# Kernel tuning notes

Hardware: AMD Instinct MI355X
Metric: run time of the kernel (lower is better)

## Reference

```python
import jax, jax.numpy as jnp
import numpy as np

B, S, TK, H, E, V, OOV = 16, 8, 400, 256, 128, 50000, 50
H2 = 2 * H


def setup_inputs() -> dict:
    key = jax.random.key(0)
    ks = jax.random.split(key, 24)
    std = 0.02
    d = {}
    d["y_t_1"] = jax.random.randint(ks[0], (B,), 0, V)
    d["h0"] = jax.random.normal(ks[1], (B, H), jnp.float32)
    d["c0"] = jax.random.normal(ks[2], (B, H), jnp.float32)
    d["encoder_output"] = jax.random.normal(ks[3], (B, S, TK, H2), jnp.float32)
    d["section_output"] = jax.random.normal(ks[4], (B, S, H2), jnp.float32)
    d["enc_padding_mask"] = jnp.ones((B, S, TK), jnp.float32)
    d["c_t_1"] = jax.random.normal(ks[5], (B, H2), jnp.float32)
    d["extra_zeros"] = jnp.zeros((B, OOV), jnp.float32)
    d["enc_batch_extend_vocab"] = jax.random.randint(ks[6], (B, S * TK), 0, V + OOV)
    d["coverage"] = jnp.zeros((B, S, TK), jnp.float32)
    d["gamma"] = jnp.ones((B, S, TK), jnp.float32)
    # learned parameters
    d["embedding"] = std * jax.random.normal(ks[7], (V, E), jnp.float32)
    d["W_xc"] = std * jax.random.normal(ks[8], (H2 + E, E), jnp.float32)
    d["b_xc"] = jnp.zeros((E,), jnp.float32)
    d["W_ih"] = std * jax.random.normal(ks[9], (E, 4 * H), jnp.float32)
    d["b_ih"] = jnp.zeros((4 * H,), jnp.float32)
    d["W_hh"] = std * jax.random.normal(ks[10], (H, 4 * H), jnp.float32)
    # pytorch init sets forget-gate bias (2nd quarter) to 1
    d["b_hh"] = jnp.zeros((4 * H,), jnp.float32).at[H:2 * H].set(1.0)
    d["Wh_sec"] = std * jax.random.normal(ks[11], (H2, H2), jnp.float32)
    d["Wd_sec"] = std * jax.random.normal(ks[12], (H2, H2), jnp.float32)
    d["bd_sec"] = jnp.zeros((H2,), jnp.float32)
    d["v_sec"] = std * jax.random.normal(ks[13], (H2, 1), jnp.float32)
    d["Wh_w"] = std * jax.random.normal(ks[14], (H2, H2), jnp.float32)
    d["Wc_w"] = std * jax.random.normal(ks[15], (H2,), jnp.float32)
    d["Wd_w"] = std * jax.random.normal(ks[16], (H2, H2), jnp.float32)
    d["bd_w"] = jnp.zeros((H2,), jnp.float32)
    d["v_w"] = std * jax.random.normal(ks[17], (H2, 1), jnp.float32)
    d["W_pgen"] = std * jax.random.normal(ks[18], (4 * H + E, 1), jnp.float32)
    d["b_pgen"] = jnp.zeros((1,), jnp.float32)
    d["W_out1"] = std * jax.random.normal(ks[19], (3 * H, H), jnp.float32)
    d["b_out1"] = jnp.zeros((H,), jnp.float32)
    d["W_out2"] = std * jax.random.normal(ks[20], (H, V), jnp.float32)
    d["b_out2"] = jnp.zeros((V,), jnp.float32)
    return d


def reference(y_t_1, h0, c0, encoder_output, section_output, enc_padding_mask,
              c_t_1, extra_zeros, enc_batch_extend_vocab, coverage, gamma,
              embedding, W_xc, b_xc, W_ih, b_ih, W_hh, b_hh,
              Wh_sec, Wd_sec, bd_sec, v_sec,
              Wh_w, Wc_w, Wd_w, bd_w, v_w,
              W_pgen, b_pgen, W_out1, b_out1, W_out2, b_out2):
    # embedding + input context projection
    emb = embedding[y_t_1]                                      # [B,E]
    x = jnp.concatenate([c_t_1, emb], axis=1) @ W_xc + b_xc     # [B,E]
    # single-step LSTM (pytorch gate order i,f,g,o)
    gates = x @ W_ih + b_ih + h0 @ W_hh + b_hh                  # [B,4H]
    i, f, g, o = jnp.split(gates, 4, axis=1)
    c = jax.nn.sigmoid(f) * c0 + jax.nn.sigmoid(i) * jnp.tanh(g)
    h = jax.nn.sigmoid(o) * jnp.tanh(c)
    s_t_hat = jnp.concatenate([h, c], axis=1)                   # [B,2H]
    # section attention -> beta [B,S]
    e_sec = jnp.tanh(section_output @ Wh_sec + (s_t_hat @ Wd_sec + bd_sec)[:, None, :])
    sc_sec = jnp.squeeze(e_sec @ v_sec, -1)                     # [B,S]
    beta = jax.nn.softmax(sc_sec, axis=1)
    beta = beta / beta.sum(axis=1, keepdims=True)
    # word attention with coverage feature
    att = encoder_output @ Wh_w + (s_t_hat @ Wd_w + bd_w)[:, None, None, :]
    att = att + coverage[..., None] * Wc_w                      # [B,S,TK,2H]
    sc_w = jnp.squeeze(jnp.tanh(att) @ v_w, -1)                 # [B,S,TK]
    ws = (beta[:, :, None] * sc_w).reshape(B, S * TK)
    mask = enc_padding_mask.reshape(B, S * TK)
    ad = jax.nn.softmax(ws, axis=1) * mask
    attn = ad / ad.sum(axis=1, keepdims=True)                   # [B,S*TK]
    c_t = jnp.einsum('bt,btn->bn', attn, encoder_output.reshape(B, S * TK, H2))
    cov = coverage + attn.reshape(B, S, TK)
    # pointer-gen gate
    p_gen = jax.nn.sigmoid(jnp.concatenate([c_t, s_t_hat, x], axis=1) @ W_pgen + b_pgen)  # [B,1]
    # output vocab distribution
    out = jnp.concatenate([h, c_t], axis=1) @ W_out1 + b_out1
    vocab_dist = jax.nn.softmax(out @ W_out2 + b_out2, axis=1)  # [B,V]
    vd = jnp.concatenate([p_gen * vocab_dist, extra_zeros], axis=1)  # [B,V+OOV]
    ad_ = (1.0 - p_gen) * attn
    rows = jnp.arange(B)[:, None]
    final_dist = vd.at[rows, enc_batch_extend_vocab].add(ad_)
    return (final_dist, h, c, c_t, attn, p_gen, cov)
```

## Files before the change

### kernel.cpp

```cpp
#include <hip/hip_runtime.h>
#include <math.h>

#define BB   16
#define SS   8
#define TKK  400
#define HH   256
#define EE   128
#define VV   50000
#define OOVV 50
#define HH2  512
#define STK  (SS*TKK)
#define VOO  (VV+OOVV)

#define OFF_X     0
#define OFF_ST    2048
#define OFF_SD    10240
#define OFF_WD    18432
#define OFF_SCSEC 26752
#define OFF_SCW   26880
#define OFF_CT    78080
#define OFF_OUT1  86272
#define OFF_PGEN  90368
#define OFF_PSUM  93520
#define OFF_BT    113040

#define O_FD   0
#define O_H    800800
#define O_C    804896
#define O_CT   808992
#define O_ATTN 817184
#define O_PGEN 868384
#define O_COV  868400

#define NLBLK 782
#define GEMM_NB 800

typedef __attribute__((ext_vector_type(8))) short bf16x8;
typedef __attribute__((ext_vector_type(4))) float f32x4;

__device__ __forceinline__ float sigm(float x){ return 1.0f/(1.0f+expf(-x)); }

__device__ __forceinline__ unsigned short f2b(float f){
  unsigned int u = __float_as_uint(f);
  unsigned int r = (u + 0x7fffu + ((u >> 16) & 1u)) >> 16;
  return (unsigned short)r;
}

__device__ __forceinline__ float wave_sum(float v){
  #pragma unroll
  for(int o=32;o>0;o>>=1) v += __shfl_xor(v,o);
  return v;
}
__device__ __forceinline__ float wave_max(float v){
  #pragma unroll
  for(int o=32;o>0;o>>=1) v = fmaxf(v,__shfl_xor(v,o));
  return v;
}

__global__ void k_pre(const float* __restrict__ Whw, unsigned short* __restrict__ Btg,
                      const int* __restrict__ y, const float* __restrict__ ct1,
                      const float* __restrict__ emb, const float* __restrict__ Wxc,
                      const float* __restrict__ bxc, float* __restrict__ ws){
  __shared__ float sm[10440];
  int bi = blockIdx.x, tid = threadIdx.x;
  if(bi < 64){
    int n0 = (bi & 7)*64, k0 = (bi >> 3)*64;
    int tx = tid & 63, ty = tid >> 6;
    #pragma unroll
    for(int it=0; it<16; it++){
      int kk = it*4 + ty;
      sm[kk*65 + tx] = Whw[(size_t)(k0+kk)*HH2 + n0 + tx];
    }
    __syncthreads();
    #pragma unroll
    for(int it=0; it<2; it++){
      int kgl = it*4 + ty;
      int kgG = (k0 >> 3) + kgl;
      union{ bf16x8 v; unsigned short u[8]; } t;
      #pragma unroll
      for(int j=0;j<8;j++) t.u[j] = f2b(sm[(kgl*8+j)*65 + tx]);
      *(bf16x8*)&Btg[((size_t)kgG*HH2 + n0 + tx)*8] = t.v;
    }
  } else if(bi < 80){
    float* cat = sm;
    float* red = sm + 10240;
    for(int f=tid; f<BB*640; f+=256){
      int b = f/640, r = f - b*640;
      cat[f] = (r < HH2) ? ct1[b*HH2 + r] : emb[(size_t)y[b]*EE + (r-HH2)];
    }
    __syncthreads();
    int c = (bi-64)*8 + (tid & 7);
    int b = (tid >> 3) & 15;
    int kh = tid >> 7;
    float acc = 0.0f;
    const float* a = &cat[b*640];
    for(int k=kh*320; k<kh*320+320; k++) acc += a[k]*Wxc[k*EE + c];
    if(kh==1) red[b*8 + (tid&7)] = acc;
    __syncthreads();
    if(kh==0) ws[OFF_X + b*EE + c] = acc + red[b*8 + (tid&7)] + bxc[c];
  } else {
    for(int f=tid; f<BB*HH2; f+=256) ws[OFF_CT + f] = 0.0f;
  }
}

__global__ void k_lstm(const float* __restrict__ h0, const float* __restrict__ c0,
                       const float* __restrict__ Wih, const float* __restrict__ bih,
                       const float* __restrict__ Whh, const float* __restrict__ bhh,
                       float* __restrict__ ws, float* __restrict__ out){
  __shared__ float xh[4*384];
  __shared__ float red[3*64*4];
  int tid = threadIdx.x;
  int jc = (blockIdx.x & 15)*16, bc = (blockIdx.x >> 4)*4;
  for(int f=tid; f<4*384; f+=256){
    int bl = f/384, r = f - bl*384;
    xh[f] = (r < EE) ? ws[OFF_X + (bc+bl)*EE + r] : h0[(bc+bl)*HH + (r-EE)];
  }
  __syncthreads();
  int jl = tid & 15, bl = (tid >> 4) & 3, kq = tid >> 6;
  int j = jc + jl, b = bc + bl;
  float a0=0.f, a1=0.f, a2=0.f, a3=0.f;
  const float* a = &xh[bl*384];
  for(int k=kq*96; k<kq*96+96; k++){
    float v = a[k];
    const float* w = (k < EE) ? &Wih[k*4*HH + j] : &Whh[(k-EE)*4*HH + j];
    a0 += v*w[0]; a1 += v*w[HH]; a2 += v*w[2*HH]; a3 += v*w[3*HH];
  }
  if(kq){
    float* r = &red[((kq-1)*64 + bl*16 + jl)*4];
    r[0]=a0; r[1]=a1; r[2]=a2; r[3]=a3;
  }
  __syncthreads();
  if(kq==0){
    #pragma unroll
    for(int p=0;p<3;p++){
      const float* r = &red[(p*64 + bl*16 + jl)*4];
      a0+=r[0]; a1+=r[1]; a2+=r[2]; a3+=r[3];
    }
    a0 += bih[j] + bhh[j];
    a1 += bih[j+HH] + bhh[j+HH];
    a2 += bih[j+2*HH] + bhh[j+2*HH];
    a3 += bih[j+3*HH] + bhh[j+3*HH];
    float c = sigm(a1)*c0[b*HH+j] + sigm(a0)*tanhf(a2);
    float h = sigm(a3)*tanhf(c);
    out[O_H + b*HH + j] = h;
    out[O_C + b*HH + j] = c;
    ws[OFF_ST + b*HH2 + j]      = h;
    ws[OFF_ST + b*HH2 + HH + j] = c;
  }
}

__global__ void k_proj(const float* __restrict__ Wdsec, const float* __restrict__ bdsec,
                       const float* __restrict__ Wdw,  const float* __restrict__ bdw,
                       float* __restrict__ ws){
  __shared__ float st[BB*HH2];
  __shared__ float red[128];
  int tid = threadIdx.x;
  for(int f=tid; f<BB*HH2; f+=256) st[f] = ws[OFF_ST + f];
  __syncthreads();
  int mi = blockIdx.x >> 6;
  int c = (blockIdx.x & 63)*8 + (tid & 7);
  int bl = (tid >> 3) & 15;
  int kq = tid >> 7;
  const float* Wm = mi ? Wdw : Wdsec;
  const float* bias = mi ? bdw : bdsec;
  int dst = mi ? OFF_WD : OFF_SD;
  float acc = 0.0f;
  const float* a = &st[bl*HH2];
  for(int k=kq*256; k<kq*256+256; k++) acc += a[k]*Wm[k*HH2 + c];
  if(kq==1) red[bl*8 + (tid&7)] = acc;
  __syncthreads();
  if(kq==0) ws[dst + bl*HH2 + c] = acc + red[bl*8 + (tid&7)] + bias[c];
}

__global__ __launch_bounds__(512, 4) void k_gemm6(
        const float* __restrict__ A, const unsigned short* __restrict__ Btg,
        const float* __restrict__ Wcw, const float* __restrict__ vw,
        const float* __restrict__ cover,
        const float* __restrict__ sec, const float* __restrict__ Whsec,
        const float* __restrict__ vsec, float* __restrict__ ws){
  __shared__ __align__(16) unsigned short smem[18432];
  int tid = threadIdx.x;
  if(blockIdx.x >= GEMM_NB){
    float* row = (float*)smem;
    float* red = row + HH2;
    int bi = blockIdx.x - GEMM_NB;
    int b = bi >> 3;
    if(tid < HH2) row[tid] = sec[(size_t)bi*HH2 + tid];
    __syncthreads();
    int col = tid;
    float acc = 0.0f;
    #pragma unroll 8
    for(int k=0;k<HH2;k++) acc += row[k]*Whsec[k*HH2 + col];
    float val = tanhf(acc + ws[OFF_SD + b*HH2 + col]) * vsec[col];
    val = wave_sum(val);
    if((tid&63)==0) red[tid>>6] = val;
    __syncthreads();
    if(tid==0){
      float s = 0.0f;
      #pragma unroll
      for(int i=0;i<8;i++) s += red[i];
      ws[OFF_SCSEC + bi] = s;
    }
    return;
  }
  unsigned short* As = smem;
  unsigned short* Bs = smem + 2048;
  int w = tid >> 6, lane = tid & 63, m = lane & 15, q = lane >> 4;
  int mk = (m >> 1) & 3;
  int rg = w >> 1, cg = w & 1;
  int row0 = blockIdx.x * 64;
  int b = blockIdx.x / 50;
  float cov[4];
  #pragma unroll
  for(int r=0;r<4;r++) cov[r] = cover[row0 + rg*16 + q*4 + r];
  f32x4 acc[16];
  #pragma unroll
  for(int j=0;j<16;j++) acc[j] = (f32x4){0.f,0.f,0.f,0.f};

  int arow = tid >> 2, akg = tid & 3;
  int bcol = tid;

  for(int rnd=0; rnd<16; rnd++){
    int k0 = rnd*32;
    if(tid < 256){
      const float4* src = (const float4*)&A[(size_t)(row0+arow)*HH2 + k0 + akg*8];
      float4 v0 = src[0], v1 = src[1];
      union{ bf16x8 v; unsigned short u[8]; } t;
      t.u[0]=f2b(v0.x); t.u[1]=f2b(v0.y); t.u[2]=f2b(v0.z); t.u[3]=f2b(v0.w);
      t.u[4]=f2b(v1.x); t.u[5]=f2b(v1.y); t.u[6]=f2b(v1.z); t.u[7]=f2b(v1.w);
      *(bf16x8*)&As[(arow*4 + (akg ^ ((arow>>1)&3)))*8] = t.v;
    }
    #pragma unroll
    for(int i=0;i<4;i++){
      bf16x8 bv = *(const bf16x8*)&Btg[((size_t)(rnd*4+i)*HH2 + bcol)*8];
      *(bf16x8*)&Bs[(bcol*4 + (i ^ ((bcol>>1)&3)))*8] = bv;
    }
    __syncthreads();
    bf16x8 af = *(bf16x8*)&As[((rg*16+m)*4 + (q ^ mk))*8];
    #pragma unroll
    for(int j=0;j<16;j++){
      int col = cg*256 + j*16 + m;
      bf16x8 bfv = *(bf16x8*)&Bs[(col*4 + (q ^ mk))*8];
      acc[j] = __builtin_amdgcn_mfma_f32_16x16x32_bf16(af, bfv, acc[j], 0,0,0);
    }
    __syncthreads();
  }
  float rsum[4] = {0,0,0,0};
  #pragma unroll
  for(int j=0;j<16;j++){
    int col = cg*256 + j*16 + m;
    float wdv = ws[OFF_WD + b*HH2 + col];
    float wcv = Wcw[col], vwv = vw[col];
    #pragma unroll
    for(int r=0;r<4;r++)
      rsum[r] += tanhf(acc[j][r] + wdv + cov[r]*wcv) * vwv;
  }
  float* rbuf = (float*)smem;
  #pragma unroll
  for(int r=0;r<4;r++){
    float v = rsum[r];
    v += __shfl_xor(v,1,16); v += __shfl_xor(v,2,16);
    v += __shfl_xor(v,4,16); v += __shfl_xor(v,8,16);
    if(m==0) rbuf[cg*64 + rg*16 + q*4 + r] = v;
  }
  __syncthreads();
  if(tid < 64) ws[OFF_SCW + row0 + tid] = rbuf[tid] + rbuf[64 + tid];
}

__global__ void k_attn(const float* __restrict__ mask, const float* __restrict__ cover,
                       float* __restrict__ ws, float* __restrict__ out){
  int b = blockIdx.x, tid = threadIdx.x;
  __shared__ float vals[STK];
  __shared__ float red[4];
  __shared__ float sc[SS];
  if(tid < SS) sc[tid] = ws[OFF_SCSEC + b*SS + tid];
  __syncthreads();
  float bm = -1e30f;
  #pragma unroll
  for(int s=0;s<SS;s++) bm = fmaxf(bm, sc[s]);
  float be[SS]; float bsum = 0.0f;
  #pragma unroll
  for(int s=0;s<SS;s++){ be[s] = expf(sc[s]-bm); bsum += be[s]; }
  #pragma unroll
  for(int s=0;s<SS;s++) be[s] /= bsum;
  int lane = tid & 63, w = tid >> 6;
  float m = -1e30f;
  for(int j=tid;j<STK;j+=256){
    float v = be[j/TKK] * ws[OFF_SCW + b*STK + j];
    vals[j] = v; m = fmaxf(m, v);
  }
  m = wave_max(m);
  if(lane==0) red[w] = m;
  __syncthreads();
  m = fmaxf(fmaxf(red[0],red[1]), fmaxf(red[2],red[3]));
  __syncthreads();
  float ssum = 0.0f;
  for(int j=tid;j<STK;j+=256){
    float e = expf(vals[j]-m) * mask[b*STK + j];
    vals[j] = e; ssum += e;
  }
  ssum = wave_sum(ssum);
  if(lane==0) red[w] = ssum;
  __syncthreads();
  float inv = 1.0f/(red[0]+red[1]+red[2]+red[3]);
  for(int j=tid;j<STK;j+=256){
    float a = vals[j]*inv;
    out[O_ATTN + b*STK + j] = a;
    out[O_COV  + b*STK + j] = cover[b*STK + j] + a;
  }
}

__global__ void k_ct(const float* __restrict__ enc, const float* __restrict__ out,
                     float* __restrict__ ws){
  int b = blockIdx.y, tid = threadIdx.x;
  __shared__ float a[64];
  int t0 = blockIdx.x*64;
  if(tid<64) a[tid] = out[O_ATTN + b*STK + t0 + tid];
  __syncthreads();
  float acc0=0.0f, acc1=0.0f;
  #pragma unroll 4
  for(int tt=0;tt<64;tt++){
    const float* row = &enc[(size_t)(b*STK + t0 + tt)*HH2];
    float av = a[tt];
    acc0 += av*row[tid];
    acc1 += av*row[256+tid];
  }
  atomicAdd(&ws[OFF_CT + b*HH2 + tid],       acc0);
  atomicAdd(&ws[OFF_CT + b*HH2 + 256 + tid], acc1);
}

__global__ void k_out1(const float* __restrict__ Wp, const float* __restrict__ bp,
                       const float* __restrict__ Wo1, const float* __restrict__ bo1,
                       float* __restrict__ ws, float* __restrict__ out){
  __shared__ float cat[BB*768];
  __shared__ float red[3*64];
  int tid = threadIdx.x;
  if(blockIdx.x == 64){
    int w = tid >> 6, lane = tid & 63;
    #pragma unroll
    for(int i=0;i<4;i++){
      int b = w*4 + i;
      float p = 0.0f;
      for(int k=lane;k<4*HH+EE;k+=64){
        float val = (k < HH2) ? ws[OFF_CT + b*HH2 + k]
                  : (k < 4*HH) ? ws[OFF_ST + b*HH2 + (k-HH2)]
                  : ws[OFF_X + b*EE + (k-4*HH)];
        p += val * Wp[k];
      }
      p = wave_sum(p);
      if(lane==0){
        float pg = sigm(p + bp[0]);
        ws[OFF_PGEN + b] = pg;
        out[O_PGEN + b]  = pg;
      }
    }
    for(int f=tid; f<BB*HH2; f+=256) out[O_CT + f] = ws[OFF_CT + f];
    return;
  }
  for(int f=tid; f<BB*768; f+=256){
    int b = f/768, r = f - b*768;
    cat[f] = (r < HH) ? ws[OFF_ST + b*HH2 + r] : ws[OFF_CT + b*HH2 + (r-HH)];
  }
  __syncthreads();
  int cl = tid & 3, bl = (tid >> 2) & 15, kq = tid >> 6;
  int c = blockIdx.x*4 + cl;
  float acc = 0.0f;
  const float* a = &cat[bl*768];
  for(int k=kq*192; k<kq*192+192; k++) acc += a[k]*Wo1[k*HH + c];
  if(kq) red[(kq-1)*64 + bl*4 + cl] = acc;
  __syncthreads();
  if(kq==0){
    acc += red[bl*4+cl] + red[64 + bl*4+cl] + red[128 + bl*4+cl];
    ws[OFF_OUT1 + bl*HH + c] = acc + bo1[c];
  }
}

__global__ void k_logits(const float* __restrict__ W2, const float* __restrict__ b2,
                         float* __restrict__ ws, float* __restrict__ out){
  int tid = threadIdx.x;
  int c = blockIdx.x*64 + (tid & 63);
  int bq = tid >> 6;
  __shared__ float o1[BB*HH];
  for(int i=tid;i<BB*HH;i+=256) o1[i] = ws[OFF_OUT1 + i];
  __syncthreads();
  bool ok = c < VV;
  float acc[4] = {0,0,0,0};
  if(ok){
    for(int k=0;k<HH;k++){
      float wv = W2[(size_t)k*VV + c];
      #pragma unroll
      for(int i=0;i<4;i++) acc[i] += o1[(bq*4+i)*HH + k]*wv;
    }
  }
  float bias = ok ? b2[c] : 0.0f;
  int lane = tid & 63;
  #pragma unroll
  for(int i=0;i<4;i++){
    float e = ok ? expf(acc[i]+bias) : 0.0f;
    if(ok) out[(size_t)(bq*4+i)*VOO + c] = e;
    float sv = wave_sum(e);
    if(lane==0) ws[OFF_PSUM + blockIdx.x*BB + bq*4 + i] = sv;
  }
}

__global__ void k_final(const float* __restrict__ xz, float* __restrict__ ws,
                        float* __restrict__ out){
  int b = blockIdx.y;
  int v = blockIdx.x*256 + threadIdx.x;
  __shared__ float red[4];
  int lane = threadIdx.x & 63, w = threadIdx.x >> 6;
  float p = 0.0f;
  for(int i=threadIdx.x;i<NLBLK;i+=256) p += ws[OFF_PSUM + i*BB + b];
  p = wave_sum(p);
  if(lane==0) red[w] = p;
  __syncthreads();
  float s = red[0]+red[1]+red[2]+red[3];
  float pg = ws[OFF_PGEN + b];
  if(v < VV)       out[(size_t)b*VOO + v] = pg * out[(size_t)b*VOO + v] / s;
  else if(v < VOO) out[(size_t)b*VOO + v] = xz[b*OOVV + (v-VV)];
}

__global__ void k_scatter(const int* __restrict__ ebev, float* __restrict__ ws,
                          float* __restrict__ out){
  int b = blockIdx.x;
  float r = 1.0f - ws[OFF_PGEN + b];
  for(int j=threadIdx.x;j<STK;j+=256){
    int idx = ebev[b*STK + j];
    atomicAdd(&out[(size_t)b*VOO + idx], r*out[O_ATTN + b*STK + j]);
  }
}

extern "C" void kernel_launch(void* const* d_in, const int* in_sizes, int n_in,
                              void* d_out, int out_size, void* d_ws, size_t ws_size,
                              hipStream_t stream){
  const int*   y     = (const int*)  d_in[0];
  const float* h0    = (const float*)d_in[1];
  const float* c0    = (const float*)d_in[2];
  const float* enc   = (const float*)d_in[3];
  const float* sec   = (const float*)d_in[4];
  const float* mask  = (const float*)d_in[5];
  const float* ct1   = (const float*)d_in[6];
  const float* xz    = (const float*)d_in[7];
  const int*   ebev  = (const int*)  d_in[8];
  const float* cover = (const float*)d_in[9];
  const float* emb   = (const float*)d_in[11];
  const float* Wxc   = (const float*)d_in[12];
  const float* bxc   = (const float*)d_in[13];
  const float* Wih   = (const float*)d_in[14];
  const float* bih   = (const float*)d_in[15];
  const float* Whh   = (const float*)d_in[16];
  const float* bhh   = (const float*)d_in[17];
  const float* Whsec = (const float*)d_in[18];
  const float* Wdsec = (const float*)d_in[19];
  const float* bdsec = (const float*)d_in[20];
  const float* vsec  = (const float*)d_in[21];
  const float* Whw   = (const float*)d_in[22];
  const float* Wcw   = (const float*)d_in[23];
  const float* Wdw   = (const float*)d_in[24];
  const float* bdw   = (const float*)d_in[25];
  const float* vw    = (const float*)d_in[26];
  const float* Wp    = (const float*)d_in[27];
  const float* bp    = (const float*)d_in[28];
  const float* Wo1   = (const float*)d_in[29];
  const float* bo1   = (const float*)d_in[30];
  const float* Wo2   = (const float*)d_in[31];
  const float* bo2   = (const float*)d_in[32];
  float* out = (float*)d_out;
  float* ws  = (float*)d_ws;
  unsigned short* Btg = (unsigned short*)(ws + OFF_BT);

  k_pre    <<<dim3(81),       dim3(256), 0, stream>>>(Whw, Btg, y, ct1, emb, Wxc, bxc, ws);
  k_lstm   <<<dim3(64),       dim3(256), 0, stream>>>(h0, c0, Wih, bih, Whh, bhh, ws, out);
  k_proj   <<<dim3(128),      dim3(256), 0, stream>>>(Wdsec, bdsec, Wdw, bdw, ws);
  k_gemm6  <<<dim3(928),      dim3(512), 0, stream>>>(enc, Btg, Wcw, vw, cover, sec, Whsec, vsec, ws);
  k_attn   <<<dim3(BB),       dim3(256), 0, stream>>>(mask, cover, ws, out);
  k_ct     <<<dim3(50,BB),    dim3(256), 0, stream>>>(enc, out, ws);
  k_out1   <<<dim3(65),       dim3(256), 0, stream>>>(Wp, bp, Wo1, bo1, ws, out);
  k_logits <<<dim3(NLBLK),    dim3(256), 0, stream>>>(Wo2, bo2, ws, out);
  k_final  <<<dim3(196,BB),   dim3(256), 0, stream>>>(xz, ws, out);
  k_scatter<<<dim3(BB),       dim3(256), 0, stream>>>(ebev, ws, out);
}
```

Before: 498.8 us.

## Pipeline attention GEMM with async LDS loads and vectorize ct and logits kernels

The attention GEMM now double-buffers pre-swizzled B tiles through direct global-to-LDS loads, and feeds A fragments from registers with a prefetch of the next k-slice. k_pre writes the weight in the swizzled layout this requires. A fast clamped exp-based tanh replaces tanhf in the GEMM epilogue. k_ct and k_logits switch to float4 loads, and k_logits uses half as many blocks with a batch-major partial-sum layout. The aim is to hide memory latency and cut instruction overhead, at the cost of a larger LDS footprint, less accurate tanh, and hand-tuned waitcnt logic that is fragile.

```diff
diff --git a/kernel.cpp b/kernel.cpp
--- a/kernel.cpp
+++ b/kernel.cpp
@@ -32,7 +32,7 @@
 #define O_PGEN 868384
 #define O_COV  868400
 
-#define NLBLK 782
+#define NLB 391
 #define GEMM_NB 800
 
 typedef __attribute__((ext_vector_type(8))) short bf16x8;
@@ -46,6 +46,12 @@
   return (unsigned short)r;
 }
 
+__device__ __forceinline__ float tanhfast(float x){
+  float cx = fminf(9.0f, fmaxf(-9.0f, x));
+  float t = __expf(2.0f*cx);
+  return (t - 1.0f) * __builtin_amdgcn_rcpf(t + 1.0f);
+}
+
 __device__ __forceinline__ float wave_sum(float v){
   #pragma unroll
   for(int o=32;o>0;o>>=1) v += __shfl_xor(v,o);
@@ -55,6 +61,18 @@
   #pragma unroll
   for(int o=32;o>0;o>>=1) v = fmaxf(v,__shfl_xor(v,o));
   return v;
+}
+
+__device__ __forceinline__ void glds16(const void* g, void* l){
+  __builtin_amdgcn_global_load_lds((const __attribute__((address_space(1))) void*)g,
+                                   (__attribute__((address_space(3))) void*)l, 16, 0, 0);
+}
+
+__device__ __forceinline__ bf16x8 cvt8(float4 a, float4 b){
+  union{ bf16x8 v; unsigned short u[8]; } t;
+  t.u[0]=f2b(a.x); t.u[1]=f2b(a.y); t.u[2]=f2b(a.z); t.u[3]=f2b(a.w);
+  t.u[4]=f2b(b.x); t.u[5]=f2b(b.y); t.u[6]=f2b(b.z); t.u[7]=f2b(b.w);
+  return t.v;
 }
 
 __global__ void k_pre(const float* __restrict__ Whw, unsigned short* __restrict__ Btg,
@@ -76,10 +94,12 @@
     for(int it=0; it<2; it++){
       int kgl = it*4 + ty;
       int kgG = (k0 >> 3) + kgl;
+      int rnd = kgG >> 2, kg = kgG & 3;
+      int col = n0 + tx;
       union{ bf16x8 v; unsigned short u[8]; } t;
       #pragma unroll
       for(int j=0;j<8;j++) t.u[j] = f2b(sm[(kgl*8+j)*65 + tx]);
-      *(bf16x8*)&Btg[((size_t)kgG*HH2 + n0 + tx)*8] = t.v;
+      *(bf16x8*)&Btg[(size_t)rnd*16384 + (size_t)(col*4 + (kg ^ ((col>>1)&3)))*8] = t.v;
     }
   } else if(bi < 80){
     float* cat = sm;
@@ -178,7 +198,7 @@
         const float* __restrict__ cover,
         const float* __restrict__ sec, const float* __restrict__ Whsec,
         const float* __restrict__ vsec, float* __restrict__ ws){
-  __shared__ __align__(16) unsigned short smem[18432];
+  __shared__ __align__(16) unsigned short smem[32768];
   int tid = threadIdx.x;
   if(blockIdx.x >= GEMM_NB){
     float* row = (float*)smem;
@@ -203,48 +223,67 @@
     }
     return;
   }
-  unsigned short* As = smem;
-  unsigned short* Bs = smem + 2048;
   int w = tid >> 6, lane = tid & 63, m = lane & 15, q = lane >> 4;
-  int mk = (m >> 1) & 3;
+  int mk = (m >> 1) & 3, sw = q ^ mk;
   int rg = w >> 1, cg = w & 1;
   int row0 = blockIdx.x * 64;
   int b = blockIdx.x / 50;
+
+  const float* arow_p = &A[(size_t)(row0 + rg*16 + m)*HH2 + q*8];
+
+  f32x4 acc[16];
+  #pragma unroll
+  for(int j=0;j<16;j++) acc[j] = (f32x4){0.f,0.f,0.f,0.f};
+
+  #define GLDSB(rr, bufsel) {                                                  \
+    const unsigned short* bsrc_ = Btg + (size_t)(rr)*16384;                    \
+    _Pragma("unroll")                                                          \
+    for(int i_=0;i_<4;i_++)                                                    \
+      glds16(bsrc_ + i_*4096 + tid*8, &smem[(bufsel)*16384 + i_*4096 + tid*8]);\
+  }
+
+  GLDSB(0, 0);
+  float4 pa0 = *(const float4*)(arow_p);
+  float4 pa1 = *(const float4*)(arow_p + 4);
+  GLDSB(1, 1);
+  asm volatile("s_waitcnt vmcnt(6)" ::: "memory");
+  __builtin_amdgcn_sched_barrier(0);
+  bf16x8 af = cvt8(pa0, pa1);
+  __builtin_amdgcn_s_barrier();
+
+  #pragma unroll
+  for(int r=0; r<16; r++){
+    if(r < 15){
+      pa0 = *(const float4*)(arow_p + (r+1)*32);
+      pa1 = *(const float4*)(arow_p + (r+1)*32 + 4);
+    }
+    __builtin_amdgcn_s_setprio(1);
+    #pragma unroll
+    for(int cf=0; cf<16; cf++){
+      int col = cg*256 + cf*16 + m;
+      bf16x8 bv = *(const bf16x8*)&smem[(size_t)(r&1)*16384 + ((size_t)col*4 + sw)*8];
+      acc[cf] = __builtin_amdgcn_mfma_f32_16x16x32_bf16(af, bv, acc[cf], 0,0,0);
+    }
+    __builtin_amdgcn_s_setprio(0);
+    if(r < 14){
+      asm volatile("s_waitcnt lgkmcnt(0)" ::: "memory");
+      __builtin_amdgcn_sched_barrier(0);
+      __builtin_amdgcn_s_barrier();
+      GLDSB(r+2, (r&1));
+    }
+    if(r < 15){
+      if(r < 14){ asm volatile("s_waitcnt vmcnt(6)" ::: "memory"); }
+      else      { asm volatile("s_waitcnt vmcnt(2)" ::: "memory"); }
+      __builtin_amdgcn_sched_barrier(0);
+      af = cvt8(pa0, pa1);
+      __builtin_amdgcn_s_barrier();
+    }
+  }
+  #undef GLDSB
+
   float cov[4];
   #pragma unroll
   for(int r=0;r<4;r++) cov[r] = cover[row0 + rg*16 + q*4 + r];
-  f32x4 acc[16];
-  #pragma unroll
-  for(int j=0;j<16;j++) acc[j] = (f32x4){0.f,0.f,0.f,0.f};
-
-  int arow = tid >> 2, akg = tid & 3;
-  int bcol = tid;
-
-  for(int rnd=0; rnd<16; rnd++){
-    int k0 = rnd*32;
-    if(tid < 256){
-      const float4* src = (const float4*)&A[(size_t)(row0+arow)*HH2 + k0 + akg*8];
-      float4 v0 = src[0], v1 = src[1];
-      union{ bf16x8 v; unsigned short u[8]; } t;
-      t.u[0]=f2b(v0.x); t.u[1]=f2b(v0.y); t.u[2]=f2b(v0.z); t.u[3]=f2b(v0.w);
-      t.u[4]=f2b(v1.x); t.u[5]=f2b(v1.y); t.u[6]=f2b(v1.z); t.u[7]=f2b(v1.w);
-      *(bf16x8*)&As[(arow*4 + (akg ^ ((arow>>1)&3)))*8] = t.v;
-    }
-    #pragma unroll
-    for(int i=0;i<4;i++){
-      bf16x8 bv = *(const bf16x8*)&Btg[((size_t)(rnd*4+i)*HH2 + bcol)*8];
-      *(bf16x8*)&Bs[(bcol*4 + (i ^ ((bcol>>1)&3)))*8] = bv;
-    }
-    __syncthreads();
-    bf16x8 af = *(bf16x8*)&As[((rg*16+m)*4 + (q ^ mk))*8];
-    #pragma unroll
-    for(int j=0;j<16;j++){
-      int col = cg*256 + j*16 + m;
-      bf16x8 bfv = *(bf16x8*)&Bs[(col*4 + (q ^ mk))*8];
-      acc[j] = __builtin_amdgcn_mfma_f32_16x16x32_bf16(af, bfv, acc[j], 0,0,0);
-    }
-    __syncthreads();
-  }
   float rsum[4] = {0,0,0,0};
   #pragma unroll
   for(int j=0;j<16;j++){
@@ -253,8 +292,9 @@
     float wcv = Wcw[col], vwv = vw[col];
     #pragma unroll
     for(int r=0;r<4;r++)
-      rsum[r] += tanhf(acc[j][r] + wdv + cov[r]*wcv) * vwv;
-  }
+      rsum[r] += tanhfast(acc[j][r] + wdv + cov[r]*wcv) * vwv;
+  }
+  __syncthreads();
   float* rbuf = (float*)smem;
   #pragma unroll
   for(int r=0;r<4;r++){
@@ -314,19 +354,29 @@
                      float* __restrict__ ws){
   int b = blockIdx.y, tid = threadIdx.x;
   __shared__ float a[64];
+  __shared__ float part[512];
   int t0 = blockIdx.x*64;
   if(tid<64) a[tid] = out[O_ATTN + b*STK + t0 + tid];
   __syncthreads();
-  float acc0=0.0f, acc1=0.0f;
-  #pragma unroll 4
-  for(int tt=0;tt<64;tt++){
-    const float* row = &enc[(size_t)(b*STK + t0 + tt)*HH2];
-    float av = a[tt];
-    acc0 += av*row[tid];
-    acc1 += av*row[256+tid];
-  }
-  atomicAdd(&ws[OFF_CT + b*HH2 + tid],       acc0);
-  atomicAdd(&ws[OFF_CT + b*HH2 + 256 + tid], acc1);
+  int c4 = tid & 127, rh = tid >> 7;
+  const float4* e4 = (const float4*)enc;
+  size_t base = ((size_t)(b*STK + t0 + rh*32))*128 + c4;
+  float4 acc = {0.f,0.f,0.f,0.f};
+  #pragma unroll 8
+  for(int rr=0; rr<32; rr++){
+    float4 v = e4[base + (size_t)rr*128];
+    float av = a[rh*32 + rr];
+    acc.x += av*v.x; acc.y += av*v.y; acc.z += av*v.z; acc.w += av*v.w;
+  }
+  if(rh) *(float4*)&part[c4*4] = acc;
+  __syncthreads();
+  if(!rh){
+    float4 o = *(const float4*)&part[c4*4];
+    atomicAdd(&ws[OFF_CT + b*HH2 + c4*4 + 0], acc.x + o.x);
+    atomicAdd(&ws[OFF_CT + b*HH2 + c4*4 + 1], acc.y + o.y);
+    atomicAdd(&ws[OFF_CT + b*HH2 + c4*4 + 2], acc.z + o.z);
+    atomicAdd(&ws[OFF_CT + b*HH2 + c4*4 + 3], acc.w + o.w);
+  }
 }
 
 __global__ void k_out1(const float* __restrict__ Wp, const float* __restrict__ bp,
@@ -378,28 +428,46 @@
 __global__ void k_logits(const float* __restrict__ W2, const float* __restrict__ b2,
                          float* __restrict__ ws, float* __restrict__ out){
   int tid = threadIdx.x;
-  int c = blockIdx.x*64 + (tid & 63);
-  int bq = tid >> 6;
   __shared__ float o1[BB*HH];
-  for(int i=tid;i<BB*HH;i+=256) o1[i] = ws[OFF_OUT1 + i];
-  __syncthreads();
-  bool ok = c < VV;
-  float acc[4] = {0,0,0,0};
+  for(int i=tid;i<BB*HH/4;i+=256)
+    ((float4*)o1)[i] = ((const float4*)&ws[OFF_OUT1])[i];
+  __syncthreads();
+  int cl = tid & 31, bq = tid >> 5;
+  int c4 = blockIdx.x*128 + cl*4;
+  bool ok = c4 < VV;
+  int b0 = bq*2, b1 = b0+1;
+  float4 acc0 = {0.f,0.f,0.f,0.f}, acc1 = {0.f,0.f,0.f,0.f};
   if(ok){
+    const float* oa = &o1[b0*HH];
+    const float* ob = &o1[b1*HH];
+    #pragma unroll 4
     for(int k=0;k<HH;k++){
-      float wv = W2[(size_t)k*VV + c];
-      #pragma unroll
-      for(int i=0;i<4;i++) acc[i] += o1[(bq*4+i)*HH + k]*wv;
-    }
-  }
-  float bias = ok ? b2[c] : 0.0f;
-  int lane = tid & 63;
-  #pragma unroll
-  for(int i=0;i<4;i++){
-    float e = ok ? expf(acc[i]+bias) : 0.0f;
-    if(ok) out[(size_t)(bq*4+i)*VOO + c] = e;
-    float sv = wave_sum(e);
-    if(lane==0) ws[OFF_PSUM + blockIdx.x*BB + bq*4 + i] = sv;
+      float4 wv = *(const float4*)&W2[(size_t)k*VV + c4];
+      float xa = oa[k], xb = ob[k];
+      acc0.x += xa*wv.x; acc0.y += xa*wv.y; acc0.z += xa*wv.z; acc0.w += xa*wv.w;
+      acc1.x += xb*wv.x; acc1.y += xb*wv.y; acc1.z += xb*wv.z; acc1.w += xb*wv.w;
+    }
+  }
+  float bv[4] = {0,0,0,0};
+  if(ok){ float4 t = *(const float4*)&b2[c4]; bv[0]=t.x; bv[1]=t.y; bv[2]=t.z; bv[3]=t.w; }
+  float a0[4] = {acc0.x, acc0.y, acc0.z, acc0.w};
+  float a1[4] = {acc1.x, acc1.y, acc1.z, acc1.w};
+  float s0 = 0.0f, s1 = 0.0f;
+  #pragma unroll
+  for(int j=0;j<4;j++){
+    float e0 = ok ? expf(a0[j]+bv[j]) : 0.0f;
+    float e1 = ok ? expf(a1[j]+bv[j]) : 0.0f;
+    if(ok){
+      out[(size_t)b0*VOO + c4 + j] = e0;
+      out[(size_t)b1*VOO + c4 + j] = e1;
+    }
+    s0 += e0; s1 += e1;
+  }
+  #pragma unroll
+  for(int o=1;o<32;o<<=1){ s0 += __shfl_xor(s0,o,32); s1 += __shfl_xor(s1,o,32); }
+  if(cl==0){
+    ws[OFF_PSUM + b0*NLB + blockIdx.x] = s0;
+    ws[OFF_PSUM + b1*NLB + blockIdx.x] = s1;
   }
 }
 
@@ -410,7 +478,7 @@
   __shared__ float red[4];
   int lane = threadIdx.x & 63, w = threadIdx.x >> 6;
   float p = 0.0f;
-  for(int i=threadIdx.x;i<NLBLK;i+=256) p += ws[OFF_PSUM + i*BB + b];
+  for(int i=threadIdx.x;i<NLB;i+=256) p += ws[OFF_PSUM + b*NLB + i];
   p = wave_sum(p);
   if(lane==0) red[w] = p;
   __syncthreads();
@@ -476,7 +544,7 @@
   k_attn   <<<dim3(BB),       dim3(256), 0, stream>>>(mask, cover, ws, out);
   k_ct     <<<dim3(50,BB),    dim3(256), 0, stream>>>(enc, out, ws);
   k_out1   <<<dim3(65),       dim3(256), 0, stream>>>(Wp, bp, Wo1, bo1, ws, out);
-  k_logits <<<dim3(NLBLK),    dim3(256), 0, stream>>>(Wo2, bo2, ws, out);
+  k_logits <<<dim3(NLB),      dim3(256), 0, stream>>>(Wo2, bo2, ws, out);
   k_final  <<<dim3(196,BB),   dim3(256), 0, stream>>>(xz, ws, out);
   k_scatter<<<dim3(BB),       dim3(256), 0, stream>>>(ebev, ws, out);
 }
```

Measured after the change: 487.6 us. 2.2% less time.
